# Performance work log

Hardware: AMD Instinct MI355X
Metric: run time of the kernel (lower is better)

## Reference

```python
import jax, jax.numpy as jnp
import numpy as np

HIDDEN = 2048
INNER = 1024
NUM_EXPERTS = 64
TOP_K = 8
T_TOKENS = 512


def setup_inputs() -> dict:
    key = jax.random.key(0)
    k_x, k_gw, k_gb, k_w1, k_w2 = jax.random.split(key, 5)
    x = jax.random.normal(k_x, (T_TOKENS, HIDDEN), dtype=jnp.float32)
    gate_w = jax.random.normal(k_gw, (NUM_EXPERTS, HIDDEN), dtype=jnp.float32) * 0.02
    gate_b = jax.random.normal(k_gb, (NUM_EXPERTS,), dtype=jnp.float32) * 0.02
    # fc1: fused gate+up, [E, 2*INNER, HIDDEN]; fc2: down, [E, HIDDEN, INNER]
    w1 = jax.random.normal(k_w1, (NUM_EXPERTS, 2 * INNER, HIDDEN), dtype=jnp.float32) * 0.02
    w2 = jax.random.normal(k_w2, (NUM_EXPERTS, HIDDEN, INNER), dtype=jnp.float32) * 0.02
    return {"x": x, "gate_w": gate_w, "gate_b": gate_b, "w1": w1, "w2": w2}


def reference(x, gate_w, gate_b, w1, w2):
    # Router: ReplicatedLinear with bias -> logits [T, E]
    logits = x @ gate_w.T + gate_b
    # FusedMoE default routing: softmax (fp32), top-k, renormalize
    probs = jax.nn.softmax(logits.astype(jnp.float32), axis=-1)
    topk_w, topk_idx = jax.lax.top_k(probs, TOP_K)          # [T, K]
    topk_w = topk_w / jnp.sum(topk_w, axis=-1, keepdims=True)
    T, E = probs.shape
    # Sparse combine weights scattered into a dense [T, E] matrix
    combine = jnp.zeros((T, E), dtype=topk_w.dtype)
    combine = combine.at[jnp.arange(T)[:, None], topk_idx].add(topk_w)
    # Expert MLPs (dense-over-experts reference; combine zeros out unrouted pairs)
    h = jnp.einsum('th,eih->tei', x, w1)                    # [T, E, 2*INNER]
    gate_h, up_h = h[..., :INNER], h[..., INNER:]
    act = jax.nn.gelu(gate_h, approximate=True) * up_h      # gelu_pytorch_tanh
    y = jnp.einsum('tei,ehi->teh', act, w2)                 # [T, E, HIDDEN]
    # Weighted scatter-combine back to tokens
    return jnp.einsum('te,teh->th', combine.astype(x.dtype), y)
```

## Files before the change

kernel.cpp:

```cpp
#include <hip/hip_runtime.h>
#include <hip/hip_bf16.h>

#define HIDDEN 2048
#define INNER  1024
#define NE     64
#define TOPK   8
#define NTOK   512

typedef float f32x4 __attribute__((ext_vector_type(4)));
typedef short bf16x8 __attribute__((ext_vector_type(8)));

static __device__ __forceinline__ unsigned short b16(float f) {
  return __builtin_bit_cast(unsigned short, __float2bfloat16(f));
}
static __device__ __forceinline__ unsigned int pk2(float lo, float hi) {
  return (unsigned)b16(lo) | ((unsigned)b16(hi) << 16);
}

static __device__ __forceinline__ void decode_ce(int flat, int& c, int& e) {
  int xcd = flat & 7, s = flat >> 3;
  c = s & 15;
  e = ((s >> 4) << 3) | xcd;
}

__global__ __launch_bounds__(256) void gating_kernel(
    const float* __restrict__ x, const float* __restrict__ gw, const float* __restrict__ gb,
    int* __restrict__ ticket, int* __restrict__ counts, int* __restrict__ offsets,
    int* __restrict__ topk_e, float* __restrict__ topk_w,
    int* __restrict__ perm_tok, int* __restrict__ invpos,
    unsigned short* __restrict__ xb) {
  const int t = blockIdx.x;
  const int tid = threadIdx.x;
  const int lane = tid & 63, w = tid >> 6;

  {
    const float4* xi = (const float4*)(x + (size_t)t * HIDDEN);
    float4 v0 = xi[tid * 2], v1 = xi[tid * 2 + 1];
    ushort4 o0, o1;
    o0.x = b16(v0.x); o0.y = b16(v0.y); o0.z = b16(v0.z); o0.w = b16(v0.w);
    o1.x = b16(v1.x); o1.y = b16(v1.y); o1.z = b16(v1.z); o1.w = b16(v1.w);
    ushort4* xo = (ushort4*)(xb + (size_t)t * HIDDEN);
    xo[tid * 2] = o0; xo[tid * 2 + 1] = o1;
  }

  const int e = tid >> 2, seg = tid & 3;
  const f32x4* gr = (const f32x4*)(gw + (size_t)e * HIDDEN);
  const f32x4* xr = (const f32x4*)(x + (size_t)t * HIDDEN);
  float acc = 0.f;
  #pragma unroll 8
  for (int k = 0; k < 128; ++k) {
    int idx = k * 4 + seg;
    f32x4 a = xr[idx], b = gr[idx];
    acc += a.x * b.x + a.y * b.y + a.z * b.z + a.w * b.w;
  }
  acc += __shfl_xor(acc, 1);
  acc += __shfl_xor(acc, 2);
  __shared__ float sP[NE];
  if (seg == 0) sP[e] = acc;
  __syncthreads();

  __shared__ float sW[TOPK];
  __shared__ int   sE[TOPK];
  if (w == 0) {
    float logit = gb[lane] + sP[lane];
    float m = logit;
    #pragma unroll
    for (int off = 32; off; off >>= 1) m = fmaxf(m, __shfl_xor(m, off));
    float p = __expf(logit - m);
    float s = p;
    #pragma unroll
    for (int off = 32; off; off >>= 1) s += __shfl_xor(s, off);
    p /= s;
    float myp = p;
    #pragma unroll
    for (int k = 0; k < TOPK; ++k) {
      float v = myp; int ei = lane;
      #pragma unroll
      for (int off = 32; off; off >>= 1) {
        float v2 = __shfl_xor(v, off); int e2 = __shfl_xor(ei, off);
        if (v2 > v || (v2 == v && e2 < ei)) { v = v2; ei = e2; }
      }
      if (lane == 0) { sW[k] = v; sE[k] = ei; }
      if (lane == ei) myp = -1.0f;
    }
  }
  __syncthreads();
  if (tid < TOPK) {
    float ss = 0.f;
    #pragma unroll
    for (int k = 0; k < TOPK; ++k) ss += sW[k];
    topk_e[t * TOPK + tid] = sE[tid];
    topk_w[t * TOPK + tid] = sW[tid] / ss;
  }

  __threadfence();
  __syncthreads();
  __shared__ int slast;
  if (tid == 0) {
    int old = atomicAdd(ticket, 1);
    slast = (old == (int)gridDim.x - 1);
  }
  __syncthreads();
  if (!slast) return;
  __threadfence();

  __shared__ int hcnt[NE], soff[NE], ccur[NE];
  if (tid < NE) hcnt[tid] = 0;
  __syncthreads();
  for (int i = tid; i < NTOK * TOPK; i += 256) atomicAdd(&hcnt[topk_e[i]], 1);
  __syncthreads();
  if (tid < NE) {
    int c = hcnt[tid];
    int s = c;
    #pragma unroll
    for (int off = 1; off < 64; off <<= 1) {
      int o = __shfl_up(s, off);
      if (tid >= off) s += o;
    }
    soff[tid] = s - c; ccur[tid] = 0;
    counts[tid] = c; offsets[tid] = s - c;
  }
  __syncthreads();
  for (int i = tid; i < NTOK * TOPK; i += 256) {
    int ee = topk_e[i];
    int p = atomicAdd(&ccur[ee], 1);
    int pos = soff[ee] + p;
    perm_tok[pos] = i >> 3;
    invpos[i] = pos;
  }
}

__global__ __launch_bounds__(512, 4) void phase1_kernel(
    const unsigned short* __restrict__ xb, const float* __restrict__ w1,
    const int* __restrict__ offsets, const int* __restrict__ counts,
    const int* __restrict__ perm_tok, unsigned short* __restrict__ act) {
  int c, e;
  decode_ce(blockIdx.x, c, e);
  const int n_e = counts[e];
  if (n_e == 0) return;
  const int off = offsets[e];
  const int tid = threadIdx.x;
  const int lane = tid & 63, wave = tid >> 6;
  const int mat = wave >> 2;
  const int wm  = (wave & 3) * 32;

  const int r32 = tid >> 4, l16 = tid & 15;
  const float* wg  = w1 + (size_t)e * (2 * INNER) * HIDDEN;
  const float* rp0 = wg + (size_t)(c * 64 + r32) * HIDDEN;
  const float* rp1 = rp0 + (size_t)32 * HIDDEN;
  const float* rp2 = rp0 + (size_t)INNER * HIDDEN;
  const float* rp3 = rp2 + (size_t)32 * HIDDEN;
  const int bidx0 = r32 * 16 + (((l16 >> 1) ^ (r32 & 7)) << 1) + (l16 & 1);

  const int ar0 = tid >> 3, ar1 = (tid >> 3) + 64;
  const int as = tid & 7;
  const int sxa = as ^ (ar0 & 7);

  __shared__ uint4 smem[2][2][128 * 8];
  __shared__ int stok[128];
  float (*sU)[68] = (float(*)[68])&smem[0][0][0];

  for (int m0 = 0; m0 < n_e; m0 += 128) {
    __syncthreads();
    if (tid < 128) {
      int idx = m0 + tid;
      stok[tid] = perm_tok[off + (idx < n_e ? idx : n_e - 1)];
    }
    __syncthreads();

    uint4 va0, va1; f32x4 vB0, vB1, vB2, vB3;
    va0 = *((const uint4*)(xb + (size_t)stok[ar0] * HIDDEN) + as);
    va1 = *((const uint4*)(xb + (size_t)stok[ar1] * HIDDEN) + as);
    vB0 = *((const f32x4*)rp0 + l16);
    vB1 = *((const f32x4*)rp1 + l16);
    vB2 = *((const f32x4*)rp2 + l16);
    vB3 = *((const f32x4*)rp3 + l16);

    f32x4 acc[2][4];
    #pragma unroll
    for (int i = 0; i < 2; ++i)
      #pragma unroll
      for (int j = 0; j < 4; ++j) acc[i][j] = (f32x4)0.f;

    for (int k0 = 0; k0 < HIDDEN; k0 += 64) {
      const int cur = (k0 >> 6) & 1;
      smem[cur][0][ar0 * 8 + sxa] = va0;
      smem[cur][0][ar1 * 8 + sxa] = va1;
      {
        uint2* b2 = (uint2*)smem[cur][1];
        b2[bidx0]        = make_uint2(pk2(vB0.x, vB0.y), pk2(vB0.z, vB0.w));
        b2[bidx0 + 512]  = make_uint2(pk2(vB1.x, vB1.y), pk2(vB1.z, vB1.w));
        b2[bidx0 + 1024] = make_uint2(pk2(vB2.x, vB2.y), pk2(vB2.z, vB2.w));
        b2[bidx0 + 1536] = make_uint2(pk2(vB3.x, vB3.y), pk2(vB3.z, vB3.w));
      }
      __syncthreads();
      int k1 = k0 + 64;
      if (k1 < HIDDEN) {
        va0 = *((const uint4*)(xb + (size_t)stok[ar0] * HIDDEN + k1) + as);
        va1 = *((const uint4*)(xb + (size_t)stok[ar1] * HIDDEN + k1) + as);
        vB0 = *((const f32x4*)(rp0 + k1) + l16);
        vB1 = *((const f32x4*)(rp1 + k1) + l16);
        vB2 = *((const f32x4*)(rp2 + k1) + l16);
        vB3 = *((const f32x4*)(rp3 + k1) + l16);
      }
      #pragma unroll
      for (int ks = 0; ks < 2; ++ks) {
        const int u = ks * 4 + (lane >> 4);
        bf16x8 af[2], bfr[4];
        #pragma unroll
        for (int mi = 0; mi < 2; ++mi) {
          int r = wm + mi * 16 + (lane & 15);
          af[mi] = __builtin_bit_cast(bf16x8, smem[cur][0][r * 8 + (u ^ (r & 7))]);
        }
        #pragma unroll
        for (int ni = 0; ni < 4; ++ni) {
          int r = mat * 64 + ni * 16 + (lane & 15);
          bfr[ni] = __builtin_bit_cast(bf16x8, smem[cur][1][r * 8 + (u ^ (r & 7))]);
        }
        #pragma unroll
        for (int mi = 0; mi < 2; ++mi)
          #pragma unroll
          for (int ni = 0; ni < 4; ++ni)
            acc[mi][ni] = __builtin_amdgcn_mfma_f32_16x16x32_bf16(af[mi], bfr[ni], acc[mi][ni], 0, 0, 0);
      }
    }

    __syncthreads();
    if (mat == 1) {
      #pragma unroll
      for (int mi = 0; mi < 2; ++mi)
        #pragma unroll
        for (int ni = 0; ni < 4; ++ni)
          #pragma unroll
          for (int r4 = 0; r4 < 4; ++r4)
            sU[wm + mi * 16 + (lane >> 4) * 4 + r4][ni * 16 + (lane & 15)] = acc[mi][ni][r4];
    }
    __syncthreads();
    if (mat == 0) {
      #pragma unroll
      for (int mi = 0; mi < 2; ++mi)
        #pragma unroll
        for (int r4 = 0; r4 < 4; ++r4) {
          int mrow = wm + mi * 16 + (lane >> 4) * 4 + r4;
          int m = m0 + mrow;
          if (m < n_e) {
            unsigned short* arow = act + (size_t)(off + m) * INNER + c * 64;
            #pragma unroll
            for (int ni = 0; ni < 4; ++ni) {
              int col = ni * 16 + (lane & 15);
              float g = acc[mi][ni][r4];
              float uu = sU[mrow][col];
              float ge = g / (1.0f + __expf(-1.5957691216057308f * (g + 0.044715f * g * g * g)));
              arow[col] = b16(ge * uu);
            }
          }
        }
    }
  }
}

__global__ __launch_bounds__(512, 4) void phase2_kernel(
    const unsigned short* __restrict__ act, const float* __restrict__ w2,
    const int* __restrict__ offsets, const int* __restrict__ counts,
    float* __restrict__ ybuf) {
  int c, e;
  decode_ce(blockIdx.x, c, e);
  const int n_e = counts[e];
  if (n_e == 0) return;
  const int off = offsets[e];
  const int tid = threadIdx.x;
  const int lane = tid & 63, wave = tid >> 6;
  const int wm = (wave & 3) * 32;
  const int wn = (wave >> 2) * 64;

  const int r32 = tid >> 4, l16 = tid & 15;
  const float* rp0 = w2 + ((size_t)e * HIDDEN + c * 128 + r32) * INNER;
  const float* rp1 = rp0 + (size_t)32 * INNER;
  const float* rp2 = rp0 + (size_t)64 * INNER;
  const float* rp3 = rp0 + (size_t)96 * INNER;
  const int bidx0 = r32 * 16 + (((l16 >> 1) ^ (r32 & 7)) << 1) + (l16 & 1);

  const int ar0 = tid >> 3, ar1 = (tid >> 3) + 64;
  const int as = tid & 7;
  const int sxa = as ^ (ar0 & 7);

  __shared__ uint4 smem[2][2][128 * 8];

  for (int m0 = 0; m0 < n_e; m0 += 128) {
    const unsigned short* a0 = act + (size_t)(off + (m0 + ar0 < n_e ? m0 + ar0 : n_e - 1)) * INNER;
    const unsigned short* a1 = act + (size_t)(off + (m0 + ar1 < n_e ? m0 + ar1 : n_e - 1)) * INNER;

    uint4 va0, va1; f32x4 vB0, vB1, vB2, vB3;
    va0 = *((const uint4*)a0 + as);
    va1 = *((const uint4*)a1 + as);
    vB0 = *((const f32x4*)rp0 + l16);
    vB1 = *((const f32x4*)rp1 + l16);
    vB2 = *((const f32x4*)rp2 + l16);
    vB3 = *((const f32x4*)rp3 + l16);

    f32x4 acc[2][4];
    #pragma unroll
    for (int i = 0; i < 2; ++i)
      #pragma unroll
      for (int j = 0; j < 4; ++j) acc[i][j] = (f32x4)0.f;

    for (int k0 = 0; k0 < INNER; k0 += 64) {
      const int cur = (k0 >> 6) & 1;
      smem[cur][0][ar0 * 8 + sxa] = va0;
      smem[cur][0][ar1 * 8 + sxa] = va1;
      {
        uint2* b2 = (uint2*)smem[cur][1];
        b2[bidx0]        = make_uint2(pk2(vB0.x, vB0.y), pk2(vB0.z, vB0.w));
        b2[bidx0 + 512]  = make_uint2(pk2(vB1.x, vB1.y), pk2(vB1.z, vB1.w));
        b2[bidx0 + 1024] = make_uint2(pk2(vB2.x, vB2.y), pk2(vB2.z, vB2.w));
        b2[bidx0 + 1536] = make_uint2(pk2(vB3.x, vB3.y), pk2(vB3.z, vB3.w));
      }
      __syncthreads();
      int k1 = k0 + 64;
      if (k1 < INNER) {
        va0 = *((const uint4*)(a0 + k1) + as);
        va1 = *((const uint4*)(a1 + k1) + as);
        vB0 = *((const f32x4*)(rp0 + k1) + l16);
        vB1 = *((const f32x4*)(rp1 + k1) + l16);
        vB2 = *((const f32x4*)(rp2 + k1) + l16);
        vB3 = *((const f32x4*)(rp3 + k1) + l16);
      }
      #pragma unroll
      for (int ks = 0; ks < 2; ++ks) {
        const int u = ks * 4 + (lane >> 4);
        bf16x8 af[2], bfr[4];
        #pragma unroll
        for (int mi = 0; mi < 2; ++mi) {
          int r = wm + mi * 16 + (lane & 15);
          af[mi] = __builtin_bit_cast(bf16x8, smem[cur][0][r * 8 + (u ^ (r & 7))]);
        }
        #pragma unroll
        for (int ni = 0; ni < 4; ++ni) {
          int r = wn + ni * 16 + (lane & 15);
          bfr[ni] = __builtin_bit_cast(bf16x8, smem[cur][1][r * 8 + (u ^ (r & 7))]);
        }
        #pragma unroll
        for (int mi = 0; mi < 2; ++mi)
          #pragma unroll
          for (int ni = 0; ni < 4; ++ni)
            acc[mi][ni] = __builtin_amdgcn_mfma_f32_16x16x32_bf16(af[mi], bfr[ni], acc[mi][ni], 0, 0, 0);
      }
    }

    #pragma unroll
    for (int mi = 0; mi < 2; ++mi)
      #pragma unroll
      for (int r4 = 0; r4 < 4; ++r4) {
        int mrow = wm + mi * 16 + (lane >> 4) * 4 + r4;
        int m = m0 + mrow;
        if (m < n_e) {
          float* orow = ybuf + (size_t)(off + m) * HIDDEN + c * 128 + wn;
          #pragma unroll
          for (int ni = 0; ni < 4; ++ni)
            orow[ni * 16 + (lane & 15)] = acc[mi][ni][r4];
        }
      }
    __syncthreads();
  }
}

__global__ __launch_bounds__(256) void combine_kernel(const float* __restrict__ ybuf,
                                                      const int* __restrict__ invpos,
                                                      const float* __restrict__ topk_w,
                                                      float* __restrict__ out) {
  int t = blockIdx.x;
  int tid = threadIdx.x;
  int col = tid * 8;
  f32x4 a0 = (f32x4)0.f, a1 = (f32x4)0.f;
  #pragma unroll
  for (int k = 0; k < TOPK; ++k) {
    int p = invpos[t * TOPK + k];
    float w = topk_w[t * TOPK + k];
    const f32x4* yr = (const f32x4*)(ybuf + (size_t)p * HIDDEN + col);
    f32x4 v0 = yr[0], v1 = yr[1];
    a0 += w * v0;
    a1 += w * v1;
  }
  f32x4* o = (f32x4*)(out + (size_t)t * HIDDEN + col);
  o[0] = a0; o[1] = a1;
}

extern "C" void kernel_launch(void* const* d_in, const int* in_sizes, int n_in,
                              void* d_out, int out_size, void* d_ws, size_t ws_size,
                              hipStream_t stream) {
  const float* x  = (const float*)d_in[0];
  const float* gw = (const float*)d_in[1];
  const float* gb = (const float*)d_in[2];
  const float* w1 = (const float*)d_in[3];
  const float* w2 = (const float*)d_in[4];
  float* out = (float*)d_out;

  char* ws = (char*)d_ws;
  int*   ticket   = (int*)(ws + 0x000);
  int*   counts   = (int*)(ws + 0x100);
  int*   offsets  = (int*)(ws + 0x200);
  int*   topk_e   = (int*)(ws + 0x1000);
  float* topk_w   = (float*)(ws + 0x5000);
  int*   perm_tok = (int*)(ws + 0x9000);
  int*   invpos   = (int*)(ws + 0xD000);
  unsigned short* xb  = (unsigned short*)(ws + 0x11000);
  unsigned short* act = (unsigned short*)(ws + 0x220000);
  float* ybuf         = (float*)(ws + 0xA20000);

  hipMemsetAsync(ticket, 0, 0x40, stream);

  gating_kernel<<<NTOK, 256, 0, stream>>>(x, gw, gb, ticket, counts, offsets,
                                          topk_e, topk_w, perm_tok, invpos, xb);
  phase1_kernel<<<1024, 512, 0, stream>>>(xb, w1, offsets, counts, perm_tok, act);
  phase2_kernel<<<1024, 512, 0, stream>>>(act, w2, offsets, counts, ybuf);
  combine_kernel<<<NTOK, 256, 0, stream>>>(ybuf, invpos, topk_w, out);
}
```

Measured before the change: 448.5 us.

## Halve N-tile per block and double grid for both expert GEMM phases

Both expert GEMM kernels now use 256-thread blocks, each covering half as many output columns (32 gate/up columns in phase1, 64 hidden columns in phase2), and the grid grows from 1024 to 2048 blocks with a 32-chunk expert decode. Wave tiling moves to 64x32 (phase1) and 32x64 (phase2) per wave, and shared memory drops to 1536 uint4 per stage. The goal is more blocks to spread the fp32 weight streaming across CUs and to raise occupancy. In exchange, every block re-loads and re-stages the same token activation rows, so activation traffic doubles, and the smaller tiles mean fewer MFMAs per byte fetched.

```diff
diff --git a/kernel.cpp b/kernel.cpp
--- a/kernel.cpp
+++ b/kernel.cpp
@@ -17,10 +17,10 @@
   return (unsigned)b16(lo) | ((unsigned)b16(hi) << 16);
 }
 
-static __device__ __forceinline__ void decode_ce(int flat, int& c, int& e) {
+static __device__ __forceinline__ void decode_ce32(int flat, int& c, int& e) {
   int xcd = flat & 7, s = flat >> 3;
-  c = s & 15;
-  e = ((s >> 4) << 3) | xcd;
+  c = s & 31;
+  e = ((s >> 5) << 3) | xcd;
 }
 
 __global__ __launch_bounds__(256) void gating_kernel(
@@ -130,35 +130,35 @@
   }
 }
 
-__global__ __launch_bounds__(512, 4) void phase1_kernel(
+__global__ __launch_bounds__(256, 3) void phase1_kernel(
     const unsigned short* __restrict__ xb, const float* __restrict__ w1,
     const int* __restrict__ offsets, const int* __restrict__ counts,
     const int* __restrict__ perm_tok, unsigned short* __restrict__ act) {
   int c, e;
-  decode_ce(blockIdx.x, c, e);
+  decode_ce32(blockIdx.x, c, e);
   const int n_e = counts[e];
   if (n_e == 0) return;
   const int off = offsets[e];
   const int tid = threadIdx.x;
   const int lane = tid & 63, wave = tid >> 6;
-  const int mat = wave >> 2;
-  const int wm  = (wave & 3) * 32;
-
-  const int r32 = tid >> 4, l16 = tid & 15;
+  const int u2 = lane >> 4, l15 = lane & 15;
+  const int mat = wave >> 1;
+  const int wm  = (wave & 1) * 64;
+
+  const int r16 = tid >> 4, l16 = tid & 15;
   const float* wg  = w1 + (size_t)e * (2 * INNER) * HIDDEN;
-  const float* rp0 = wg + (size_t)(c * 64 + r32) * HIDDEN;
-  const float* rp1 = rp0 + (size_t)32 * HIDDEN;
-  const float* rp2 = rp0 + (size_t)INNER * HIDDEN;
-  const float* rp3 = rp2 + (size_t)32 * HIDDEN;
-  const int bidx0 = r32 * 16 + (((l16 >> 1) ^ (r32 & 7)) << 1) + (l16 & 1);
-
-  const int ar0 = tid >> 3, ar1 = (tid >> 3) + 64;
-  const int as = tid & 7;
-  const int sxa = as ^ (ar0 & 7);
-
-  __shared__ uint4 smem[2][2][128 * 8];
+  const float* rp0 = wg + (size_t)(c * 32 + r16) * HIDDEN;
+  const float* rp1 = rp0 + (size_t)16 * HIDDEN;
+  const float* rp2 = wg + (size_t)(INNER + c * 32 + r16) * HIDDEN;
+  const float* rp3 = rp2 + (size_t)16 * HIDDEN;
+  const int bidx0 = r16 * 16 + (((l16 >> 1) ^ (r16 & 7)) << 1) + (l16 & 1);
+
+  const int ar = tid >> 3, as = tid & 7;
+  const int sxa = as ^ (ar & 7);
+
+  __shared__ uint4 smem[2][1536];
   __shared__ int stok[128];
-  float (*sU)[68] = (float(*)[68])&smem[0][0][0];
+  float (*sU)[36] = (float(*)[36])&smem[0][0];
 
   for (int m0 = 0; m0 < n_e; m0 += 128) {
     __syncthreads();
@@ -168,59 +168,71 @@
     }
     __syncthreads();
 
-    uint4 va0, va1; f32x4 vB0, vB1, vB2, vB3;
-    va0 = *((const uint4*)(xb + (size_t)stok[ar0] * HIDDEN) + as);
-    va1 = *((const uint4*)(xb + (size_t)stok[ar1] * HIDDEN) + as);
-    vB0 = *((const f32x4*)rp0 + l16);
-    vB1 = *((const f32x4*)rp1 + l16);
-    vB2 = *((const f32x4*)rp2 + l16);
-    vB3 = *((const f32x4*)rp3 + l16);
-
-    f32x4 acc[2][4];
-    #pragma unroll
-    for (int i = 0; i < 2; ++i)
-      #pragma unroll
-      for (int j = 0; j < 4; ++j) acc[i][j] = (f32x4)0.f;
+    const unsigned short* xr0 = xb + (size_t)stok[ar] * HIDDEN;
+    const unsigned short* xr1 = xb + (size_t)stok[ar + 32] * HIDDEN;
+    const unsigned short* xr2 = xb + (size_t)stok[ar + 64] * HIDDEN;
+    const unsigned short* xr3 = xb + (size_t)stok[ar + 96] * HIDDEN;
+
+    uint4 va0 = *((const uint4*)xr0 + as);
+    uint4 va1 = *((const uint4*)xr1 + as);
+    uint4 va2 = *((const uint4*)xr2 + as);
+    uint4 va3 = *((const uint4*)xr3 + as);
+    f32x4 vB0 = *((const f32x4*)rp0 + l16);
+    f32x4 vB1 = *((const f32x4*)rp1 + l16);
+    f32x4 vB2 = *((const f32x4*)rp2 + l16);
+    f32x4 vB3 = *((const f32x4*)rp3 + l16);
+
+    f32x4 acc[4][2];
+    #pragma unroll
+    for (int i = 0; i < 4; ++i)
+      #pragma unroll
+      for (int j = 0; j < 2; ++j) acc[i][j] = (f32x4)0.f;
 
     for (int k0 = 0; k0 < HIDDEN; k0 += 64) {
       const int cur = (k0 >> 6) & 1;
-      smem[cur][0][ar0 * 8 + sxa] = va0;
-      smem[cur][0][ar1 * 8 + sxa] = va1;
+      uint4* A = smem[cur];
+      A[ar * 8 + sxa]          = va0;
+      A[(ar + 32) * 8 + sxa]   = va1;
+      A[(ar + 64) * 8 + sxa]   = va2;
+      A[(ar + 96) * 8 + sxa]   = va3;
       {
-        uint2* b2 = (uint2*)smem[cur][1];
-        b2[bidx0]        = make_uint2(pk2(vB0.x, vB0.y), pk2(vB0.z, vB0.w));
-        b2[bidx0 + 512]  = make_uint2(pk2(vB1.x, vB1.y), pk2(vB1.z, vB1.w));
-        b2[bidx0 + 1024] = make_uint2(pk2(vB2.x, vB2.y), pk2(vB2.z, vB2.w));
-        b2[bidx0 + 1536] = make_uint2(pk2(vB3.x, vB3.y), pk2(vB3.z, vB3.w));
+        uint2* bb = (uint2*)(smem[cur] + 1024);
+        bb[bidx0]       = make_uint2(pk2(vB0.x, vB0.y), pk2(vB0.z, vB0.w));
+        bb[bidx0 + 256] = make_uint2(pk2(vB1.x, vB1.y), pk2(vB1.z, vB1.w));
+        bb[bidx0 + 512] = make_uint2(pk2(vB2.x, vB2.y), pk2(vB2.z, vB2.w));
+        bb[bidx0 + 768] = make_uint2(pk2(vB3.x, vB3.y), pk2(vB3.z, vB3.w));
       }
       __syncthreads();
       int k1 = k0 + 64;
       if (k1 < HIDDEN) {
-        va0 = *((const uint4*)(xb + (size_t)stok[ar0] * HIDDEN + k1) + as);
-        va1 = *((const uint4*)(xb + (size_t)stok[ar1] * HIDDEN + k1) + as);
+        va0 = *((const uint4*)(xr0 + k1) + as);
+        va1 = *((const uint4*)(xr1 + k1) + as);
+        va2 = *((const uint4*)(xr2 + k1) + as);
+        va3 = *((const uint4*)(xr3 + k1) + as);
         vB0 = *((const f32x4*)(rp0 + k1) + l16);
         vB1 = *((const f32x4*)(rp1 + k1) + l16);
         vB2 = *((const f32x4*)(rp2 + k1) + l16);
         vB3 = *((const f32x4*)(rp3 + k1) + l16);
       }
+      const uint4* Bq = smem[cur] + 1024;
       #pragma unroll
       for (int ks = 0; ks < 2; ++ks) {
-        const int u = ks * 4 + (lane >> 4);
-        bf16x8 af[2], bfr[4];
-        #pragma unroll
-        for (int mi = 0; mi < 2; ++mi) {
-          int r = wm + mi * 16 + (lane & 15);
-          af[mi] = __builtin_bit_cast(bf16x8, smem[cur][0][r * 8 + (u ^ (r & 7))]);
-        }
-        #pragma unroll
-        for (int ni = 0; ni < 4; ++ni) {
-          int r = mat * 64 + ni * 16 + (lane & 15);
-          bfr[ni] = __builtin_bit_cast(bf16x8, smem[cur][1][r * 8 + (u ^ (r & 7))]);
-        }
-        #pragma unroll
-        for (int mi = 0; mi < 2; ++mi)
+        const int u = ks * 4 + u2;
+        bf16x8 af[4], bfr[2];
+        #pragma unroll
+        for (int mi = 0; mi < 4; ++mi) {
+          int r = wm + mi * 16 + l15;
+          af[mi] = __builtin_bit_cast(bf16x8, A[r * 8 + (u ^ (r & 7))]);
+        }
+        #pragma unroll
+        for (int ni = 0; ni < 2; ++ni) {
+          int r = mat * 32 + ni * 16 + l15;
+          bfr[ni] = __builtin_bit_cast(bf16x8, Bq[r * 8 + (u ^ (r & 7))]);
+        }
+        #pragma unroll
+        for (int mi = 0; mi < 4; ++mi)
           #pragma unroll
-          for (int ni = 0; ni < 4; ++ni)
+          for (int ni = 0; ni < 2; ++ni)
             acc[mi][ni] = __builtin_amdgcn_mfma_f32_16x16x32_bf16(af[mi], bfr[ni], acc[mi][ni], 0, 0, 0);
       }
     }
@@ -228,26 +240,26 @@
     __syncthreads();
     if (mat == 1) {
       #pragma unroll
-      for (int mi = 0; mi < 2; ++mi)
-        #pragma unroll
-        for (int ni = 0; ni < 4; ++ni)
+      for (int mi = 0; mi < 4; ++mi)
+        #pragma unroll
+        for (int ni = 0; ni < 2; ++ni)
           #pragma unroll
           for (int r4 = 0; r4 < 4; ++r4)
-            sU[wm + mi * 16 + (lane >> 4) * 4 + r4][ni * 16 + (lane & 15)] = acc[mi][ni][r4];
+            sU[wm + mi * 16 + u2 * 4 + r4][ni * 16 + l15] = acc[mi][ni][r4];
     }
     __syncthreads();
     if (mat == 0) {
       #pragma unroll
-      for (int mi = 0; mi < 2; ++mi)
+      for (int mi = 0; mi < 4; ++mi)
         #pragma unroll
         for (int r4 = 0; r4 < 4; ++r4) {
-          int mrow = wm + mi * 16 + (lane >> 4) * 4 + r4;
+          int mrow = wm + mi * 16 + u2 * 4 + r4;
           int m = m0 + mrow;
           if (m < n_e) {
-            unsigned short* arow = act + (size_t)(off + m) * INNER + c * 64;
+            unsigned short* arow = act + (size_t)(off + m) * INNER + c * 32;
             #pragma unroll
-            for (int ni = 0; ni < 4; ++ni) {
-              int col = ni * 16 + (lane & 15);
+            for (int ni = 0; ni < 2; ++ni) {
+              int col = ni * 16 + l15;
               float g = acc[mi][ni][r4];
               float uu = sU[mrow][col];
               float ge = g / (1.0f + __expf(-1.5957691216057308f * (g + 0.044715f * g * g * g)));
@@ -259,44 +271,46 @@
   }
 }
 
-__global__ __launch_bounds__(512, 4) void phase2_kernel(
+__global__ __launch_bounds__(256, 3) void phase2_kernel(
     const unsigned short* __restrict__ act, const float* __restrict__ w2,
     const int* __restrict__ offsets, const int* __restrict__ counts,
     float* __restrict__ ybuf) {
   int c, e;
-  decode_ce(blockIdx.x, c, e);
+  decode_ce32(blockIdx.x, c, e);
   const int n_e = counts[e];
   if (n_e == 0) return;
   const int off = offsets[e];
   const int tid = threadIdx.x;
   const int lane = tid & 63, wave = tid >> 6;
-  const int wm = (wave & 3) * 32;
-  const int wn = (wave >> 2) * 64;
-
-  const int r32 = tid >> 4, l16 = tid & 15;
-  const float* rp0 = w2 + ((size_t)e * HIDDEN + c * 128 + r32) * INNER;
-  const float* rp1 = rp0 + (size_t)32 * INNER;
-  const float* rp2 = rp0 + (size_t)64 * INNER;
-  const float* rp3 = rp0 + (size_t)96 * INNER;
-  const int bidx0 = r32 * 16 + (((l16 >> 1) ^ (r32 & 7)) << 1) + (l16 & 1);
-
-  const int ar0 = tid >> 3, ar1 = (tid >> 3) + 64;
-  const int as = tid & 7;
-  const int sxa = as ^ (ar0 & 7);
-
-  __shared__ uint4 smem[2][2][128 * 8];
+  const int u2 = lane >> 4, l15 = lane & 15;
+  const int wm = wave * 32;
+
+  const int r16 = tid >> 4, l16 = tid & 15;
+  const float* rp0 = w2 + ((size_t)e * HIDDEN + c * 64 + r16) * INNER;
+  const float* rp1 = rp0 + (size_t)16 * INNER;
+  const float* rp2 = rp0 + (size_t)32 * INNER;
+  const float* rp3 = rp0 + (size_t)48 * INNER;
+  const int bidx0 = r16 * 16 + (((l16 >> 1) ^ (r16 & 7)) << 1) + (l16 & 1);
+
+  const int ar = tid >> 3, as = tid & 7;
+  const int sxa = as ^ (ar & 7);
+
+  __shared__ uint4 smem[2][1536];
 
   for (int m0 = 0; m0 < n_e; m0 += 128) {
-    const unsigned short* a0 = act + (size_t)(off + (m0 + ar0 < n_e ? m0 + ar0 : n_e - 1)) * INNER;
-    const unsigned short* a1 = act + (size_t)(off + (m0 + ar1 < n_e ? m0 + ar1 : n_e - 1)) * INNER;
-
-    uint4 va0, va1; f32x4 vB0, vB1, vB2, vB3;
-    va0 = *((const uint4*)a0 + as);
-    va1 = *((const uint4*)a1 + as);
-    vB0 = *((const f32x4*)rp0 + l16);
-    vB1 = *((const f32x4*)rp1 + l16);
-    vB2 = *((const f32x4*)rp2 + l16);
-    vB3 = *((const f32x4*)rp3 + l16);
+    const unsigned short* a0 = act + (size_t)(off + (m0 + ar      < n_e ? m0 + ar      : n_e - 1)) * INNER;
+    const unsigned short* a1 = act + (size_t)(off + (m0 + ar + 32 < n_e ? m0 + ar + 32 : n_e - 1)) * INNER;
+    const unsigned short* a2 = act + (size_t)(off + (m0 + ar + 64 < n_e ? m0 + ar + 64 : n_e - 1)) * INNER;
+    const unsigned short* a3 = act + (size_t)(off + (m0 + ar + 96 < n_e ? m0 + ar + 96 : n_e - 1)) * INNER;
+
+    uint4 va0 = *((const uint4*)a0 + as);
+    uint4 va1 = *((const uint4*)a1 + as);
+    uint4 va2 = *((const uint4*)a2 + as);
+    uint4 va3 = *((const uint4*)a3 + as);
+    f32x4 vB0 = *((const f32x4*)rp0 + l16);
+    f32x4 vB1 = *((const f32x4*)rp1 + l16);
+    f32x4 vB2 = *((const f32x4*)rp2 + l16);
+    f32x4 vB3 = *((const f32x4*)rp3 + l16);
 
     f32x4 acc[2][4];
     #pragma unroll
@@ -306,38 +320,44 @@
 
     for (int k0 = 0; k0 < INNER; k0 += 64) {
       const int cur = (k0 >> 6) & 1;
-      smem[cur][0][ar0 * 8 + sxa] = va0;
-      smem[cur][0][ar1 * 8 + sxa] = va1;
+      uint4* A = smem[cur];
+      A[ar * 8 + sxa]          = va0;
+      A[(ar + 32) * 8 + sxa]   = va1;
+      A[(ar + 64) * 8 + sxa]   = va2;
+      A[(ar + 96) * 8 + sxa]   = va3;
       {
-        uint2* b2 = (uint2*)smem[cur][1];
-        b2[bidx0]        = make_uint2(pk2(vB0.x, vB0.y), pk2(vB0.z, vB0.w));
-        b2[bidx0 + 512]  = make_uint2(pk2(vB1.x, vB1.y), pk2(vB1.z, vB1.w));
-        b2[bidx0 + 1024] = make_uint2(pk2(vB2.x, vB2.y), pk2(vB2.z, vB2.w));
-        b2[bidx0 + 1536] = make_uint2(pk2(vB3.x, vB3.y), pk2(vB3.z, vB3.w));
+        uint2* bb = (uint2*)(smem[cur] + 1024);
+        bb[bidx0]       = make_uint2(pk2(vB0.x, vB0.y), pk2(vB0.z, vB0.w));
+        bb[bidx0 + 256] = make_uint2(pk2(vB1.x, vB1.y), pk2(vB1.z, vB1.w));
+        bb[bidx0 + 512] = make_uint2(pk2(vB2.x, vB2.y), pk2(vB2.z, vB2.w));
+        bb[bidx0 + 768] = make_uint2(pk2(vB3.x, vB3.y), pk2(vB3.z, vB3.w));
       }
       __syncthreads();
       int k1 = k0 + 64;
       if (k1 < INNER) {
         va0 = *((const uint4*)(a0 + k1) + as);
         va1 = *((const uint4*)(a1 + k1) + as);
+        va2 = *((const uint4*)(a2 + k1) + as);
+        va3 = *((const uint4*)(a3 + k1) + as);
         vB0 = *((const f32x4*)(rp0 + k1) + l16);
         vB1 = *((const f32x4*)(rp1 + k1) + l16);
         vB2 = *((const f32x4*)(rp2 + k1) + l16);
         vB3 = *((const f32x4*)(rp3 + k1) + l16);
       }
+      const uint4* Bq = smem[cur] + 1024;
       #pragma unroll
       for (int ks = 0; ks < 2; ++ks) {
-        const int u = ks * 4 + (lane >> 4);
+        const int u = ks * 4 + u2;
         bf16x8 af[2], bfr[4];
         #pragma unroll
         for (int mi = 0; mi < 2; ++mi) {
-          int r = wm + mi * 16 + (lane & 15);
-          af[mi] = __builtin_bit_cast(bf16x8, smem[cur][0][r * 8 + (u ^ (r & 7))]);
+          int r = wm + mi * 16 + l15;
+          af[mi] = __builtin_bit_cast(bf16x8, A[r * 8 + (u ^ (r & 7))]);
         }
         #pragma unroll
         for (int ni = 0; ni < 4; ++ni) {
-          int r = wn + ni * 16 + (lane & 15);
-          bfr[ni] = __builtin_bit_cast(bf16x8, smem[cur][1][r * 8 + (u ^ (r & 7))]);
+          int r = ni * 16 + l15;
+          bfr[ni] = __builtin_bit_cast(bf16x8, Bq[r * 8 + (u ^ (r & 7))]);
         }
         #pragma unroll
         for (int mi = 0; mi < 2; ++mi)
@@ -351,13 +371,13 @@
     for (int mi = 0; mi < 2; ++mi)
       #pragma unroll
       for (int r4 = 0; r4 < 4; ++r4) {
-        int mrow = wm + mi * 16 + (lane >> 4) * 4 + r4;
+        int mrow = wm + mi * 16 + u2 * 4 + r4;
         int m = m0 + mrow;
         if (m < n_e) {
-          float* orow = ybuf + (size_t)(off + m) * HIDDEN + c * 128 + wn;
+          float* orow = ybuf + (size_t)(off + m) * HIDDEN + c * 64;
           #pragma unroll
           for (int ni = 0; ni < 4; ++ni)
-            orow[ni * 16 + (lane & 15)] = acc[mi][ni][r4];
+            orow[ni * 16 + l15] = acc[mi][ni][r4];
         }
       }
     __syncthreads();
@@ -411,7 +431,7 @@
 
   gating_kernel<<<NTOK, 256, 0, stream>>>(x, gw, gb, ticket, counts, offsets,
                                           topk_e, topk_w, perm_tok, invpos, xb);
-  phase1_kernel<<<1024, 512, 0, stream>>>(xb, w1, offsets, counts, perm_tok, act);
-  phase2_kernel<<<1024, 512, 0, stream>>>(act, w2, offsets, counts, ybuf);
+  phase1_kernel<<<2048, 256, 0, stream>>>(xb, w1, offsets, counts, perm_tok, act);
+  phase2_kernel<<<2048, 256, 0, stream>>>(act, w2, offsets, counts, ybuf);
   combine_kernel<<<NTOK, 256, 0, stream>>>(ybuf, invpos, topk_w, out);
 }
```

Result: no change. 440.7 us (-1.7%).
